# Performance work log

Measured on AMD Instinct MI355X. Metric: run time of the kernel, lower is better.

The kernel has to match this reference:

```python
import jax, jax.numpy as jnp
import numpy as np
import math

D_MODEL = 1024
N_HEADS = 16
D_K = 64
D_V = 64
B = 4
S = 1024


def setup_inputs() -> dict:
    key = jax.random.key(0)
    ks = jax.random.split(key, 11)
    # xavier-ish init scale for projections
    s_in = 1.0 / math.sqrt(D_MODEL)
    return {
        "queries": jax.random.normal(ks[0], (B, S, D_MODEL), jnp.float32),
        "keys": jax.random.normal(ks[1], (B, S, D_MODEL), jnp.float32),
        "values": jax.random.normal(ks[2], (B, S, D_MODEL), jnp.float32),
        "Wq": jax.random.normal(ks[3], (D_MODEL, N_HEADS * D_K), jnp.float32) * s_in,
        "bq": jnp.zeros((N_HEADS * D_K,), jnp.float32),
        "Wk": jax.random.normal(ks[4], (D_MODEL, N_HEADS * D_K), jnp.float32) * s_in,
        "bk": jnp.zeros((N_HEADS * D_K,), jnp.float32),
        "Wv": jax.random.normal(ks[5], (D_MODEL, N_HEADS * D_V), jnp.float32) * s_in,
        "bv": jnp.zeros((N_HEADS * D_V,), jnp.float32),
        "Wo": jax.random.normal(ks[6], (N_HEADS * D_V, D_MODEL), jnp.float32) * (1.0 / math.sqrt(N_HEADS * D_V)),
        "bo": jnp.zeros((D_MODEL,), jnp.float32),
    }


def reference(queries, keys, values, Wq, bq, Wk, bk, Wv, bv, Wo, bo):
    Bq, Sq, _ = queries.shape
    Sk = keys.shape[1]
    scale = 1.0 / math.sqrt(D_K)
    # projections -> [B, S, H, d]
    q = (queries @ Wq + bq).reshape(Bq, Sq, N_HEADS, D_K)
    k = (keys @ Wk + bk).reshape(Bq, Sk, N_HEADS, D_K)
    v = (values @ Wv + bv).reshape(Bq, Sk, N_HEADS, D_V)
    # scaled dot-product attention: scores [B, H, Sq, Sk]
    scores = jnp.einsum("bqhd,bkhd->bhqk", q, k) * scale
    attn = jax.nn.softmax(scores, axis=-1)
    # weighted values -> [B, Sq, H*D_V]
    out = jnp.einsum("bhqk,bkhd->bqhd", attn, v).reshape(Bq, Sq, N_HEADS * D_V)
    return out @ Wo + bo
```

## Files before the change

### kernel.cpp

```cpp
#include <hip/hip_runtime.h>

typedef __bf16 bf16;
typedef __attribute__((ext_vector_type(4))) __bf16 bf16x4;
typedef __attribute__((ext_vector_type(8))) __bf16 bf16x8;
typedef __attribute__((ext_vector_type(4))) float f32x4;

#define D_MODEL 1024
#define NH      16
#define DHEAD   64
#define BATCH   4
#define SLEN    1024
#define MROWS   (BATCH * SLEN)
#define C2SCALE 0.18033688f
#define SOFTMAX_OFF 20.0f

__device__ __forceinline__ void async_load16(const void* g, void* l) {
  __builtin_amdgcn_global_load_lds(
      (const __attribute__((address_space(1))) unsigned int*)g,
      (__attribute__((address_space(3))) unsigned int*)l,
      16, 0, 0);
}

#define WAITCNT(N) asm volatile("s_waitcnt vmcnt(" #N ")" ::: "memory")

__global__ __launch_bounds__(256) void prep_kernel(
    const float* __restrict__ x0, const float* __restrict__ x1, const float* __restrict__ x2,
    bf16* __restrict__ y0, bf16* __restrict__ y1, bf16* __restrict__ y2, int n,
    const float* __restrict__ w0, const float* __restrict__ w1,
    const float* __restrict__ w2, const float* __restrict__ w3,
    bf16* __restrict__ t0, bf16* __restrict__ t1,
    bf16* __restrict__ t2, bf16* __restrict__ t3)
{
  __shared__ float tile[32][33];
  const int bid = blockIdx.x;
  if (bid < 3 * 4096) {
    const int z = bid >> 12, bx = bid & 4095;
    const float* x; bf16* y;
    switch (z) {
      case 0: x = x0; y = y0; break;
      case 1: x = x1; y = y1; break;
      default: x = x2; y = y2; break;
    }
    int i = (bx * 256 + threadIdx.x) * 4;
    if (i + 3 < n) {
      f32x4 v = *(const f32x4*)(x + i);
      bf16x4 o;
      o[0] = (bf16)v[0]; o[1] = (bf16)v[1]; o[2] = (bf16)v[2]; o[3] = (bf16)v[3];
      *(bf16x4*)(y + i) = o;
    }
  } else {
    const int r = bid - 3 * 4096;
    const int z = r >> 10, rr = r & 1023;
    const float* W; bf16* T;
    switch (z) {
      case 0: W = w0; T = t0; break;
      case 1: W = w1; T = t1; break;
      case 2: W = w2; T = t2; break;
      default: W = w3; T = t3; break;
    }
    const int bx = (rr & 31) * 32, by = (rr >> 5) * 32;
    const int tx = threadIdx.x & 31, ty = threadIdx.x >> 5;
    #pragma unroll
    for (int i = 0; i < 32; i += 8)
      tile[ty + i][tx] = W[(size_t)(by + ty + i) * 1024 + bx + tx];
    __syncthreads();
    #pragma unroll
    for (int i = 0; i < 32; i += 8)
      T[(size_t)(bx + ty + i) * 1024 + by + tx] = (bf16)tile[tx][ty + i];
  }
}

__global__ __launch_bounds__(256) void proj_qkv_kernel(
    const bf16* __restrict__ Xq, const bf16* __restrict__ Xk, const bf16* __restrict__ Xv,
    const bf16* __restrict__ WqT, const bf16* __restrict__ WkT, const bf16* __restrict__ WvT,
    const float* __restrict__ bq, const float* __restrict__ bk, const float* __restrict__ bv,
    bf16* __restrict__ Qh, bf16* __restrict__ Kh, bf16* __restrict__ VTo)
{
  __shared__ bf16 As[2][128 * 32];
  __shared__ bf16 Bs[2][128 * 32];

  const int g = blockIdx.x + (blockIdx.y << 3) + (blockIdx.z << 8);
  const int xcd = g & 7, local = g >> 3;
  const int grp = xcd * 12 + (local >> 3);
  const int z  = grp >> 5;
  const int by = grp & 31;
  const int bx = local & 7;

  const bf16 *A, *BT; const float* bias;
  switch (z) {
    case 0: A = Xq; BT = WqT; bias = bq; break;
    case 1: A = Xk; BT = WkT; bias = bk; break;
    default: A = Xv; BT = WvT; bias = bv; break;
  }
  const int t = threadIdx.x;
  const int wave = t >> 6, lane = t & 63;
  const int quad = lane >> 4, l16 = lane & 15;
  const int wr = wave >> 1, wc = wave & 1;
  const int bM = by * 128, bN = bx * 128;

  f32x4 acc[4][4] = {};

  auto stage = [&](int buf, int k0) {
    #pragma unroll
    for (int i = 0; i < 2; ++i) {
      const int c = i * 256 + t;
      const int p = c >> 3;
      const int sl = (c & 7) ^ (p & 7);
      const int row = 2 * p + (sl >> 2), cg = sl & 3;
      async_load16(A  + (size_t)(bM + row) * D_MODEL + k0 + cg * 8,
                   &As[buf][(i * 256 + wave * 64) * 8]);
      async_load16(BT + (size_t)(bN + row) * D_MODEL + k0 + cg * 8,
                   &Bs[buf][(i * 256 + wave * 64) * 8]);
    }
  };
  auto compute = [&](int buf) {
    bf16x8 af[4], bfr[4];
    #pragma unroll
    for (int i = 0; i < 4; ++i) {
      const int r = wr * 64 + i * 16 + l16;
      const int p = r >> 1, slot = (((r & 1) << 2) + quad) ^ (p & 7);
      af[i] = *(const bf16x8*)((const char*)&As[buf][0] + p * 128 + slot * 16);
    }
    #pragma unroll
    for (int j = 0; j < 4; ++j) {
      const int r = wc * 64 + j * 16 + l16;
      const int p = r >> 1, slot = (((r & 1) << 2) + quad) ^ (p & 7);
      bfr[j] = *(const bf16x8*)((const char*)&Bs[buf][0] + p * 128 + slot * 16);
    }
    #pragma unroll
    for (int i = 0; i < 4; ++i)
      #pragma unroll
      for (int j = 0; j < 4; ++j)
        acc[i][j] = __builtin_amdgcn_mfma_f32_16x16x32_bf16(af[i], bfr[j], acc[i][j], 0, 0, 0);
  };

  stage(0, 0);
  int buf = 0;
  for (int step = 0; step < 32; ++step) {
    if (step < 31) {
      stage(buf ^ 1, (step + 1) * 32);
      WAITCNT(4);
    } else {
      WAITCNT(0);
    }
    __builtin_amdgcn_s_barrier();
    compute(buf);
    __builtin_amdgcn_s_barrier();
    buf ^= 1;
  }

  #pragma unroll
  for (int j = 0; j < 4; ++j) {
    const int col = bN + wc * 64 + j * 16 + l16;
    const int h = col >> 6, d = col & 63;
    const float bv_ = bias[col];
    #pragma unroll
    for (int i = 0; i < 4; ++i) {
      const int row0 = bM + wr * 64 + i * 16 + quad * 4;
      const int b = row0 >> 10, s0 = row0 & 1023;
      if (z == 0) {
        bf16* dst = Qh + ((size_t)(b * NH + h) * SLEN) * DHEAD;
        #pragma unroll
        for (int r = 0; r < 4; ++r)
          dst[(size_t)(s0 + r) * DHEAD + d] = (bf16)((acc[i][j][r] + bv_) * C2SCALE);
      } else if (z == 1) {
        bf16* dst = Kh + ((size_t)(b * NH + h) * SLEN) * DHEAD;
        #pragma unroll
        for (int r = 0; r < 4; ++r)
          dst[(size_t)(s0 + r) * DHEAD + d] = (bf16)(acc[i][j][r] + bv_);
      } else {
        bf16x4 pv;
        #pragma unroll
        for (int r = 0; r < 4; ++r) pv[r] = (bf16)(acc[i][j][r] + bv_);
        *(bf16x4*)(VTo + ((size_t)(b * NH + h) * DHEAD + d) * SLEN + s0) = pv;
      }
    }
  }
}

__global__ __launch_bounds__(256) void out_proj_kernel(
    const bf16* __restrict__ AO, const bf16* __restrict__ WoT,
    const float* __restrict__ bo, float* __restrict__ Out)
{
  __shared__ bf16 As[2][64 * 32];
  __shared__ bf16 Bs[2][128 * 32];

  const int g = blockIdx.x + (blockIdx.y << 3);
  const int xcd = g & 7, local = g >> 3;
  const int grp = xcd * 8 + (local >> 3);
  const int bx = local & 7;

  const int t = threadIdx.x;
  const int wave = t >> 6, lane = t & 63;
  const int quad = lane >> 4, l16 = lane & 15;
  const int wr = wave >> 1, wc = wave & 1;
  const int bM = grp * 64, bN = bx * 128;

  f32x4 acc[2][4] = {};

  auto stage = [&](int buf, int k0) {
    {
      const int c = t;
      const int p = c >> 3;
      const int sl = (c & 7) ^ (p & 7);
      const int row = 2 * p + (sl >> 2), cg = sl & 3;
      async_load16(AO + (size_t)(bM + row) * D_MODEL + k0 + cg * 8,
                   &As[buf][(wave * 64) * 8]);
    }
    #pragma unroll
    for (int i = 0; i < 2; ++i) {
      const int c = i * 256 + t;
      const int p = c >> 3;
      const int sl = (c & 7) ^ (p & 7);
      const int row = 2 * p + (sl >> 2), cg = sl & 3;
      async_load16(WoT + (size_t)(bN + row) * D_MODEL + k0 + cg * 8,
                   &Bs[buf][(i * 256 + wave * 64) * 8]);
    }
  };
  auto compute = [&](int buf) {
    bf16x8 af[2], bfr[4];
    #pragma unroll
    for (int i = 0; i < 2; ++i) {
      const int r = wr * 32 + i * 16 + l16;
      const int p = r >> 1, slot = (((r & 1) << 2) + quad) ^ (p & 7);
      af[i] = *(const bf16x8*)((const char*)&As[buf][0] + p * 128 + slot * 16);
    }
    #pragma unroll
    for (int j = 0; j < 4; ++j) {
      const int r = wc * 64 + j * 16 + l16;
      const int p = r >> 1, slot = (((r & 1) << 2) + quad) ^ (p & 7);
      bfr[j] = *(const bf16x8*)((const char*)&Bs[buf][0] + p * 128 + slot * 16);
    }
    #pragma unroll
    for (int i = 0; i < 2; ++i)
      #pragma unroll
      for (int j = 0; j < 4; ++j)
        acc[i][j] = __builtin_amdgcn_mfma_f32_16x16x32_bf16(af[i], bfr[j], acc[i][j], 0, 0, 0);
  };

  stage(0, 0);
  int buf = 0;
  for (int step = 0; step < 32; ++step) {
    if (step < 31) {
      stage(buf ^ 1, (step + 1) * 32);
      WAITCNT(3);
    } else {
      WAITCNT(0);
    }
    __builtin_amdgcn_s_barrier();
    compute(buf);
    __builtin_amdgcn_s_barrier();
    buf ^= 1;
  }

  #pragma unroll
  for (int j = 0; j < 4; ++j) {
    const int col = bN + wc * 64 + j * 16 + l16;
    const float bv_ = bo[col];
    #pragma unroll
    for (int i = 0; i < 2; ++i) {
      const int row0 = bM + wr * 32 + i * 16 + quad * 4;
      #pragma unroll
      for (int r = 0; r < 4; ++r)
        Out[(size_t)(row0 + r) * D_MODEL + col] = acc[i][j][r] + bv_;
    }
  }
}

__global__ __launch_bounds__(256) void attn_kernel(
    const bf16* __restrict__ Q, const bf16* __restrict__ K,
    const bf16* __restrict__ VT, bf16* __restrict__ O)
{
  __shared__ bf16 Kl[2][64 * 64];
  __shared__ bf16 Vl[2][64 * 64];
  __shared__ bf16 Ps[4][2 * 16 * 72];

  const int lin = blockIdx.x + (blockIdx.y << 3);
  const int xcd = lin & 7, rr = lin >> 3;
  const int bh = xcd * 8 + (rr >> 3);
  const int qBase = (rr & 7) << 7;
  const int b = bh >> 4, h = bh & 15;

  const int t = threadIdx.x;
  const int wave = t >> 6, lane = t & 63;
  const int quad = lane >> 4, l16 = lane & 15;
  const int swz = (l16 & 7) << 4;

  const bf16* qb = Q  + (size_t)bh * SLEN * DHEAD;
  const bf16* kb = K  + (size_t)bh * SLEN * DHEAD;
  const bf16* vb = VT + (size_t)bh * DHEAD * SLEN;

  const int qRow0 = qBase + wave * 32;

  bf16x8 qa[2][2];
  #pragma unroll
  for (int g = 0; g < 2; ++g) {
    const bf16* qr = qb + (size_t)(qRow0 + g * 16 + l16) * DHEAD;
    qa[g][0] = *(const bf16x8*)(qr + quad * 8);
    qa[g][1] = *(const bf16x8*)(qr + 32 + quad * 8);
  }

  f32x4 o_acc[2][4] = {};
  float rs[2][4] = {};
  bf16* Pw = Ps[wave];

  auto stageTile = [&](int buf, int tile) {
    const int kt = tile * 64;
    #pragma unroll
    for (int i = 0; i < 2; ++i) {
      const int c = i * 256 + t;
      const int row = c >> 3;
      const int sl = ((c & 7) ^ (row & 7)) * 8;
      async_load16(kb + (size_t)(kt + row) * DHEAD + sl,
                   &Kl[buf][(i * 256 + wave * 64) * 8]);
      async_load16(vb + (size_t)row * SLEN + kt + sl,
                   &Vl[buf][(i * 256 + wave * 64) * 8]);
    }
  };

  auto tileCompute = [&](int buf) {
    const char* kB = (const char*)&Kl[buf][0];
    const char* vB = (const char*)&Vl[buf][0];

    bf16x8 kf0[4], kf1[4];
    #pragma unroll
    for (int jn = 0; jn < 4; ++jn) {
      const int rb = (jn * 16 + l16) * 128;
      kf0[jn] = *(const bf16x8*)(kB + rb + ((quad * 16) ^ swz));
      kf1[jn] = *(const bf16x8*)(kB + rb + ((64 + quad * 16) ^ swz));
    }

    f32x4 s[2][4] = {};
    __builtin_amdgcn_s_setprio(1);
    #pragma unroll
    for (int jn = 0; jn < 4; ++jn) {
      s[0][jn] = __builtin_amdgcn_mfma_f32_16x16x32_bf16(qa[0][0], kf0[jn], s[0][jn], 0, 0, 0);
      s[0][jn] = __builtin_amdgcn_mfma_f32_16x16x32_bf16(qa[0][1], kf1[jn], s[0][jn], 0, 0, 0);
      s[1][jn] = __builtin_amdgcn_mfma_f32_16x16x32_bf16(qa[1][0], kf0[jn], s[1][jn], 0, 0, 0);
      s[1][jn] = __builtin_amdgcn_mfma_f32_16x16x32_bf16(qa[1][1], kf1[jn], s[1][jn], 0, 0, 0);
    }
    __builtin_amdgcn_s_setprio(0);

    #pragma unroll
    for (int g = 0; g < 2; ++g) {
      bf16* ps = Pw + g * (16 * 72);
      #pragma unroll
      for (int jn = 0; jn < 4; ++jn)
        #pragma unroll
        for (int r = 0; r < 4; ++r) {
          float p = __builtin_amdgcn_exp2f(s[g][jn][r] - SOFTMAX_OFF);
          rs[g][r] += p;
          ps[(quad * 4 + r) * 72 + jn * 16 + l16] = (bf16)p;
        }
    }

    bf16x8 pa[2][2];
    #pragma unroll
    for (int g = 0; g < 2; ++g) {
      const bf16* ps = Pw + g * (16 * 72);
      pa[g][0] = *(const bf16x8*)(&ps[l16 * 72 + quad * 8]);
      pa[g][1] = *(const bf16x8*)(&ps[l16 * 72 + 32 + quad * 8]);
    }

    bf16x8 vf0[4], vf1[4];
    #pragma unroll
    for (int jn = 0; jn < 4; ++jn) {
      const int rb = (jn * 16 + l16) * 128;
      vf0[jn] = *(const bf16x8*)(vB + rb + ((quad * 16) ^ swz));
      vf1[jn] = *(const bf16x8*)(vB + rb + ((64 + quad * 16) ^ swz));
    }

    __builtin_amdgcn_s_setprio(1);
    #pragma unroll
    for (int jn = 0; jn < 4; ++jn) {
      o_acc[0][jn] = __builtin_amdgcn_mfma_f32_16x16x32_bf16(pa[0][0], vf0[jn], o_acc[0][jn], 0, 0, 0);
      o_acc[0][jn] = __builtin_amdgcn_mfma_f32_16x16x32_bf16(pa[0][1], vf1[jn], o_acc[0][jn], 0, 0, 0);
      o_acc[1][jn] = __builtin_amdgcn_mfma_f32_16x16x32_bf16(pa[1][0], vf0[jn], o_acc[1][jn], 0, 0, 0);
      o_acc[1][jn] = __builtin_amdgcn_mfma_f32_16x16x32_bf16(pa[1][1], vf1[jn], o_acc[1][jn], 0, 0, 0);
    }
    __builtin_amdgcn_s_setprio(0);
  };

  stageTile(0, 0);
  int buf = 0;
  for (int tt = 0; tt < 16; ++tt) {
    if (tt < 15) {
      stageTile(buf ^ 1, tt + 1);
      WAITCNT(4);
    } else {
      WAITCNT(0);
    }
    __builtin_amdgcn_s_barrier();
    tileCompute(buf);
    __builtin_amdgcn_s_barrier();
    buf ^= 1;
  }

  #pragma unroll
  for (int g = 0; g < 2; ++g)
    #pragma unroll
    for (int r = 0; r < 4; ++r) {
      float v = rs[g][r];
      #pragma unroll
      for (int off = 1; off < 16; off <<= 1)
        v += __shfl_xor(v, off);
      rs[g][r] = v;
    }

  #pragma unroll
  for (int g = 0; g < 2; ++g)
    #pragma unroll
    for (int r = 0; r < 4; ++r) {
      const float inv = 1.0f / rs[g][r];
      const int row = qRow0 + g * 16 + quad * 4 + r;
      bf16* op = O + ((size_t)b * SLEN + row) * D_MODEL + h * DHEAD;
      #pragma unroll
      for (int jn = 0; jn < 4; ++jn)
        op[jn * 16 + l16] = (bf16)(o_acc[g][jn][r] * inv);
    }
}

extern "C" void kernel_launch(void* const* d_in, const int* in_sizes, int n_in,
                              void* d_out, int out_size, void* d_ws, size_t ws_size,
                              hipStream_t stream) {
  const float* xq = (const float*)d_in[0];
  const float* xk = (const float*)d_in[1];
  const float* xv = (const float*)d_in[2];
  const float* Wq = (const float*)d_in[3];
  const float* bq = (const float*)d_in[4];
  const float* Wk = (const float*)d_in[5];
  const float* bk = (const float*)d_in[6];
  const float* Wv = (const float*)d_in[7];
  const float* bv = (const float*)d_in[8];
  const float* Wo = (const float*)d_in[9];
  const float* bo = (const float*)d_in[10];
  float* out = (float*)d_out;

  const size_t NX = (size_t)MROWS * D_MODEL;
  const size_t NW = (size_t)D_MODEL * D_MODEL;

  char* ws = (char*)d_ws;
  bf16* AO  = (bf16*)ws;  ws += NX * 2;
  bf16* WoT = (bf16*)ws;  ws += NW * 2;
  bf16* Xq  = (bf16*)ws;  ws += NX * 2;
  bf16* Xk  = (bf16*)ws;  ws += NX * 2;
  bf16* Xv  = (bf16*)ws;  ws += NX * 2;
  bf16* WqT = (bf16*)ws;  ws += NW * 2;
  bf16* WkT = (bf16*)ws;  ws += NW * 2;
  bf16* WvT = (bf16*)ws;  ws += NW * 2;
  bf16* Qh  = (bf16*)ws;  ws += NX * 2;
  bf16* Kh  = (bf16*)ws;  ws += NX * 2;
  bf16* VTb = (bf16*)ws;  ws += NX * 2;

  prep_kernel<<<dim3(3 * 4096 + 4 * 1024), 256, 0, stream>>>(
      xq, xk, xv, Xq, Xk, Xv, (int)NX, Wq, Wk, Wv, Wo, WqT, WkT, WvT, WoT);
  proj_qkv_kernel<<<dim3(8, 32, 3), 256, 0, stream>>>(Xq, Xk, Xv, WqT, WkT, WvT, bq, bk, bv, Qh, Kh, VTb);
  attn_kernel<<<dim3(8, 64), 256, 0, stream>>>(Qh, Kh, VTb, AO);
  out_proj_kernel<<<dim3(8, 64), 256, 0, stream>>>(AO, WoT, bo, out);
}
```

Before: 209.0 us.

## Triple-buffer GEMM LDS stages and drop second barrier; vectorize weight transpose stores

Both projection GEMMs now use three LDS buffers rotated in an unrolled loop, so the barrier after each compute step can go: the buffer being overwritten is two stages old. This cuts barriers per K-step in half and lets the next load overlap the current compute. The weight transpose now writes four bf16 values per thread as one vector store instead of scalar stores. The cost is 50% more LDS per block, which may reduce occupancy, and the change depends on the prefetch distance keeping the reused buffer safe without the extra barrier.

```diff
diff --git a/kernel.cpp b/kernel.cpp
--- a/kernel.cpp
+++ b/kernel.cpp
@@ -64,9 +64,11 @@
     for (int i = 0; i < 32; i += 8)
       tile[ty + i][tx] = W[(size_t)(by + ty + i) * 1024 + bx + tx];
     __syncthreads();
-    #pragma unroll
-    for (int i = 0; i < 32; i += 8)
-      T[(size_t)(bx + ty + i) * 1024 + by + tx] = (bf16)tile[tx][ty + i];
+    const int orow = threadIdx.x >> 3, cg = threadIdx.x & 7;
+    bf16x4 o;
+    #pragma unroll
+    for (int i = 0; i < 4; ++i) o[i] = (bf16)tile[cg * 4 + i][orow];
+    *(bf16x4*)(T + (size_t)(bx + orow) * 1024 + by + cg * 4) = o;
   }
 }
 
@@ -76,8 +78,8 @@
     const float* __restrict__ bq, const float* __restrict__ bk, const float* __restrict__ bv,
     bf16* __restrict__ Qh, bf16* __restrict__ Kh, bf16* __restrict__ VTo)
 {
-  __shared__ bf16 As[2][128 * 32];
-  __shared__ bf16 Bs[2][128 * 32];
+  __shared__ bf16 As[3][128 * 32];
+  __shared__ bf16 Bs[3][128 * 32];
 
   const int g = blockIdx.x + (blockIdx.y << 3) + (blockIdx.z << 8);
   const int xcd = g & 7, local = g >> 3;
@@ -135,19 +137,14 @@
   };
 
   stage(0, 0);
-  int buf = 0;
-  for (int step = 0; step < 32; ++step) {
-    if (step < 31) {
-      stage(buf ^ 1, (step + 1) * 32);
-      WAITCNT(4);
-    } else {
-      WAITCNT(0);
-    }
-    __builtin_amdgcn_s_barrier();
-    compute(buf);
-    __builtin_amdgcn_s_barrier();
-    buf ^= 1;
-  }
+  for (int it = 0; it < 10; ++it) {
+    const int s = it * 3;
+    stage(1, (s + 1) * 32); WAITCNT(4); __builtin_amdgcn_s_barrier(); compute(0);
+    stage(2, (s + 2) * 32); WAITCNT(4); __builtin_amdgcn_s_barrier(); compute(1);
+    stage(0, (s + 3) * 32); WAITCNT(4); __builtin_amdgcn_s_barrier(); compute(2);
+  }
+  stage(1, 31 * 32); WAITCNT(4); __builtin_amdgcn_s_barrier(); compute(0);
+  WAITCNT(0); __builtin_amdgcn_s_barrier(); compute(1);
 
   #pragma unroll
   for (int j = 0; j < 4; ++j) {
@@ -182,8 +179,8 @@
     const bf16* __restrict__ AO, const bf16* __restrict__ WoT,
     const float* __restrict__ bo, float* __restrict__ Out)
 {
-  __shared__ bf16 As[2][64 * 32];
-  __shared__ bf16 Bs[2][128 * 32];
+  __shared__ bf16 As[3][64 * 32];
+  __shared__ bf16 Bs[3][128 * 32];
 
   const int g = blockIdx.x + (blockIdx.y << 3);
   const int xcd = g & 7, local = g >> 3;
@@ -239,19 +236,14 @@
   };
 
   stage(0, 0);
-  int buf = 0;
-  for (int step = 0; step < 32; ++step) {
-    if (step < 31) {
-      stage(buf ^ 1, (step + 1) * 32);
-      WAITCNT(3);
-    } else {
-      WAITCNT(0);
-    }
-    __builtin_amdgcn_s_barrier();
-    compute(buf);
-    __builtin_amdgcn_s_barrier();
-    buf ^= 1;
-  }
+  for (int it = 0; it < 10; ++it) {
+    const int s = it * 3;
+    stage(1, (s + 1) * 32); WAITCNT(3); __builtin_amdgcn_s_barrier(); compute(0);
+    stage(2, (s + 2) * 32); WAITCNT(3); __builtin_amdgcn_s_barrier(); compute(1);
+    stage(0, (s + 3) * 32); WAITCNT(3); __builtin_amdgcn_s_barrier(); compute(2);
+  }
+  stage(1, 31 * 32); WAITCNT(3); __builtin_amdgcn_s_barrier(); compute(0);
+  WAITCNT(0); __builtin_amdgcn_s_barrier(); compute(1);
 
   #pragma unroll
   for (int j = 0; j < 4; ++j) {
```

Measured after the change: 209.0 us. About the same (+0.0%).
